# Kernel tuning notes

Hardware: AMD Instinct MI355X
Metric: run time of the kernel (lower is better)

## Reference

```python
import jax, jax.numpy as jnp
import numpy as np

EMBED_DIM = 1024
NUM_HEADS = 16
HEAD_DIM = EMBED_DIM // NUM_HEADS
B, N = 4, 2048


def setup_inputs() -> dict:
    key = jax.random.key(0)
    k = jax.random.split(key, 5)
    s = 1.0 / np.sqrt(EMBED_DIM)
    return {
        "x": jax.random.normal(k[0], (B, N, EMBED_DIM), dtype=jnp.float32),
        "W_qkv": jax.random.uniform(k[1], (EMBED_DIM, 3 * EMBED_DIM), jnp.float32, -s, s),
        "b_qkv": jax.random.uniform(k[2], (3 * EMBED_DIM,), jnp.float32, -s, s),
        "W_proj": jax.random.uniform(k[3], (EMBED_DIM, EMBED_DIM), jnp.float32, -s, s),
        "b_proj": jax.random.uniform(k[4], (EMBED_DIM,), jnp.float32, -s, s),
    }


def reference(x, W_qkv, b_qkv, W_proj, b_proj):
    b, n, c = x.shape
    qkv = x @ W_qkv + b_qkv                       # [B,N,3C]
    qkv = qkv.reshape(b, n, 3, NUM_HEADS, HEAD_DIM)
    q = qkv[:, :, 0].transpose(0, 2, 1, 3)        # [B,H,N,D]
    k = qkv[:, :, 1].transpose(0, 2, 1, 3)
    v = qkv[:, :, 2].transpose(0, 2, 1, 3)
    scale = 1.0 / np.sqrt(HEAD_DIM).astype(np.float32)
    scores = jnp.einsum("bhqd,bhkd->bhqk", q, k) * scale
    attn = jax.nn.softmax(scores, axis=-1)
    out = jnp.einsum("bhqk,bhkd->bhqd", attn, v)  # [B,H,N,D]
    out = out.transpose(0, 2, 1, 3).reshape(b, n, c)
    return out @ W_proj + b_proj
```

## Files before the change

### kernel.cpp

```cpp
#include <hip/hip_runtime.h>
#include <math.h>


typedef __bf16 bf16x8 __attribute__((ext_vector_type(8)));
typedef float f32x4 __attribute__((ext_vector_type(4)));

#define EMBED 1024
#define NHEAD 16
#define BATCH 4
#define SEQ 2048
#define M_TOT 8192
#define QKV_N 3072
#define QSCALE 0.18033688011112042f

__device__ __forceinline__ ushort f2bf(float f) {
  union { float f; unsigned u; } x; x.f = f;
  unsigned r = x.u + 0x7FFFu + ((x.u >> 16) & 1u);
  return (ushort)(r >> 16);
}

__device__ __forceinline__ uint cvt2bf(float a, float b) {
#if __has_builtin(__builtin_amdgcn_cvt_pk_bf16_f32)
  typedef __bf16 bf16x2 __attribute__((ext_vector_type(2)));
  union { bf16x2 v; uint u; } c;
  c.v = __builtin_amdgcn_cvt_pk_bf16_f32(a, b);
  return c.u;
#else
  return (uint)f2bf(a) | ((uint)f2bf(b) << 16);
#endif
}

__device__ __forceinline__ f32x4 mfma16(bf16x8 a, bf16x8 b, f32x4 c) {
  return __builtin_amdgcn_mfma_f32_16x16x32_bf16(a, b, c, 0, 0, 0);
}

__device__ __forceinline__ void gl2lds16(const void* g, void* l) {
  __builtin_amdgcn_global_load_lds(
      (const __attribute__((address_space(1))) unsigned int*)g,
      (__attribute__((address_space(3))) unsigned int*)l, 16, 0, 0);
}

__global__ __launch_bounds__(256) void cvt_f32_bf16(
    const float* __restrict__ in, ushort* __restrict__ out) {
  int i = (blockIdx.x * 256 + threadIdx.x) * 4;
  float4 v = *reinterpret_cast<const float4*>(&in[i]);
  uint2 w = {cvt2bf(v.x, v.y), cvt2bf(v.z, v.w)};
  *reinterpret_cast<uint2*>(&out[i]) = w;
}

__global__ __launch_bounds__(256) void transpose_to_bf16(
    const float* __restrict__ in, ushort* __restrict__ out, int Kd, int Nd) {
  __shared__ float tile[64][65];
  const int t = threadIdx.x;
  const int n0 = blockIdx.x * 64, k0 = blockIdx.y * 64;
#pragma unroll
  for (int i = 0; i < 16; ++i) {
    int e = t + 256 * i;
    int kr = e >> 6, nc = e & 63;
    tile[kr][nc] = in[(size_t)(k0 + kr) * Nd + n0 + nc];
  }
  __syncthreads();
#pragma unroll
  for (int i = 0; i < 16; ++i) {
    int e = t + 256 * i;
    int nr = e >> 6, kc = e & 63;
    out[(size_t)(n0 + nr) * Kd + k0 + kc] = f2bf(tile[kc][nr]);
  }
}

__global__ __launch_bounds__(256) void gemm_bf16(
    const ushort* __restrict__ A, const ushort* __restrict__ Bt,
    const float* __restrict__ bias, void* __restrict__ Cout,
    ushort* __restrict__ vtgout, int M, int N, int K, int mode) {
  __shared__ ushort As[128 * 32];
  __shared__ ushort Bs[128 * 32];
  const int t = threadIdx.x;
  const int wave = t >> 6, lane = t & 63;
  const int lane15 = lane & 15, quad = lane >> 4;
  const int m0 = blockIdx.y * 128, n0 = blockIdx.x * 128;
  const int wm = (wave >> 1) * 64, wn = (wave & 1) * 64;

  int srow[2], scol[2], sdst[2];
#pragma unroll
  for (int j = 0; j < 2; ++j) {
    int c = (j * 4 + wave) * 64 + lane;
    int row = c >> 2;
    scol[j] = (((c & 3) ^ ((row >> 1) & 3)) * 8);
    srow[j] = row;
    sdst[j] = (j * 4 + wave) * 512;
  }
  const int swG = (lane15 >> 1) & 3;

  f32x4 acc[4][4] = {};

  for (int k0 = 0; k0 < K; k0 += 32) {
#pragma unroll
    for (int j = 0; j < 2; ++j) {
      gl2lds16(&A[(size_t)(m0 + srow[j]) * K + k0 + scol[j]], &As[sdst[j]]);
      gl2lds16(&Bt[(size_t)(n0 + srow[j]) * K + k0 + scol[j]], &Bs[sdst[j]]);
    }
    __syncthreads();

    bf16x8 af[4], bfr[4];
#pragma unroll
    for (int ms = 0; ms < 4; ++ms)
      af[ms] = *reinterpret_cast<const bf16x8*>(
          &As[(wm + ms * 16 + lane15) * 32 + ((quad ^ swG) * 8)]);
#pragma unroll
    for (int ns = 0; ns < 4; ++ns)
      bfr[ns] = *reinterpret_cast<const bf16x8*>(
          &Bs[(wn + ns * 16 + lane15) * 32 + ((quad ^ swG) * 8)]);
#pragma unroll
    for (int ms = 0; ms < 4; ++ms)
#pragma unroll
      for (int ns = 0; ns < 4; ++ns)
        acc[ms][ns] = mfma16(af[ms], bfr[ns], acc[ms][ns]);
    __syncthreads();
  }

  if (mode == 0) {
    float* out = (float*)Cout;
#pragma unroll
    for (int ns = 0; ns < 4; ++ns) {
      int col = n0 + wn + ns * 16 + lane15;
      float bv = bias[col];
#pragma unroll
      for (int ms = 0; ms < 4; ++ms)
#pragma unroll
        for (int r = 0; r < 4; ++r) {
          int row = m0 + wm + ms * 16 + quad * 4 + r;
          out[(size_t)row * N + col] = acc[ms][ns][r] + bv;
        }
    }
  } else {
    ushort* qk = (ushort*)Cout;
#pragma unroll
    for (int ns = 0; ns < 4; ++ns) {
      int col = n0 + wn + ns * 16 + lane15;
      float bv = bias[col];
      if (col < 2048) {
        float sc = (col < 1024) ? QSCALE : 1.0f;
#pragma unroll
        for (int ms = 0; ms < 4; ++ms) {
          int row = m0 + wm + ms * 16 + quad * 4;
          uint u01 = cvt2bf((acc[ms][ns][0] + bv) * sc, (acc[ms][ns][1] + bv) * sc);
          uint u23 = cvt2bf((acc[ms][ns][2] + bv) * sc, (acc[ms][ns][3] + bv) * sc);
          qk[(size_t)(row + 0) * 2048 + col] = (ushort)u01;
          qk[(size_t)(row + 1) * 2048 + col] = (ushort)(u01 >> 16);
          qk[(size_t)(row + 2) * 2048 + col] = (ushort)u23;
          qk[(size_t)(row + 3) * 2048 + col] = (ushort)(u23 >> 16);
        }
      } else {
        int dp = col - 2048;
#pragma unroll
        for (int ms = 0; ms < 4; ++ms) {
          int row = m0 + wm + ms * 16 + quad * 4;
          int b = row >> 11, seq = row & 2047;
          uint2 w = {cvt2bf(acc[ms][ns][0] + bv, acc[ms][ns][1] + bv),
                     cvt2bf(acc[ms][ns][2] + bv, acc[ms][ns][3] + bv)};
          *reinterpret_cast<uint2*>(
              &vtgout[((size_t)(b * 1024 + dp) << 11) + seq]) = w;
        }
      }
    }
  }
}

#define APD 72
#define QG 4

__global__ __launch_bounds__(256, 2) void attn_kernel(
    const ushort* __restrict__ qk, const ushort* __restrict__ vtg,
    ushort* __restrict__ out) {
  __shared__ ushort Ks[2][4096];
  __shared__ ushort Vt[2][4096];
  __shared__ ushort Ps[4][16 * APD];

  const int t = threadIdx.x;
  const int wave = t >> 6, lane = t & 63;
  const int lane15 = lane & 15, quad = lane >> 4;
  const int bh = blockIdx.x, qg = blockIdx.y;
  const int b = bh >> 4, h = bh & 15;
  const size_t boff = (size_t)b * SEQ * 2048;

  int sdst[2];
  const ushort* kptr[2];
  const ushort* vptr[2];
#pragma unroll
  for (int j = 0; j < 2; ++j) {
    int lg = (j * 4 + wave) * 64 + lane;
    int row = lg >> 3;
    int col = ((lg & 7) ^ (row & 7)) * 8;
    sdst[j] = (j * 4 + wave) * 512;
    kptr[j] = qk + boff + (size_t)row * 2048 + 1024 + h * 64 + col;
    vptr[j] = vtg + ((size_t)(b * 1024 + h * 64 + row) << 11) + col;
  }

  bf16x8 qf[QG][2];
#pragma unroll
  for (int g = 0; g < QG; ++g) {
    size_t qoff =
        boff + (size_t)(qg * 256 + g * 64 + wave * 16 + lane15) * 2048 + h * 64;
    qf[g][0] = *reinterpret_cast<const bf16x8*>(&qk[qoff + quad * 8]);
    qf[g][1] = *reinterpret_cast<const bf16x8*>(&qk[qoff + 32 + quad * 8]);
  }

  bf16x8 ones;
#pragma unroll
  for (int j = 0; j < 8; ++j) ones[j] = (__bf16)1.0f;

  f32x4 O[QG][4] = {};
  f32x4 lacc[QG] = {};
  const int sw = lane15 & 7;
  ushort* ps = Ps[wave];

#pragma unroll
  for (int j = 0; j < 2; ++j) {
    gl2lds16(kptr[j], &Ks[0][sdst[j]]);
    gl2lds16(vptr[j], &Vt[0][sdst[j]]);
  }
  __syncthreads();

  for (int kt = 0; kt < SEQ / 64; ++kt) {
    const int cur = kt & 1, nxt = cur ^ 1;
    if (kt < SEQ / 64 - 1) {
#pragma unroll
      for (int j = 0; j < 2; ++j) {
        gl2lds16(kptr[j] + (size_t)(kt + 1) * 64 * 2048, &Ks[nxt][sdst[j]]);
        gl2lds16(vptr[j] + (kt + 1) * 64, &Vt[nxt][sdst[j]]);
      }
    }

    bf16x8 kf[4][2], vf[2][4];
#pragma unroll
    for (int nsub = 0; nsub < 4; ++nsub) {
      const int kr = (nsub * 16 + lane15) * 64;
      kf[nsub][0] = *reinterpret_cast<const bf16x8*>(
          &Ks[cur][kr + ((quad ^ sw) * 8)]);
      kf[nsub][1] = *reinterpret_cast<const bf16x8*>(
          &Ks[cur][kr + (((quad + 4) ^ sw) * 8)]);
    }
#pragma unroll
    for (int kk = 0; kk < 2; ++kk)
#pragma unroll
      for (int dsub = 0; dsub < 4; ++dsub) {
        int d = dsub * 16 + lane15;
        vf[kk][dsub] = *reinterpret_cast<const bf16x8*>(
            &Vt[cur][d * 64 + (((kk * 4 + quad) ^ sw) * 8)]);
      }

#pragma unroll
    for (int g = 0; g < QG; ++g) {
      f32x4 st[4];
#pragma unroll
      for (int nsub = 0; nsub < 4; ++nsub) {
        f32x4 a = {-32.0f, -32.0f, -32.0f, -32.0f};
        a = mfma16(kf[nsub][0], qf[g][0], a);
        a = mfma16(kf[nsub][1], qf[g][1], a);
        st[nsub] = a;
      }
#pragma unroll
      for (int nsub = 0; nsub < 4; ++nsub) {
        uint2 w = {cvt2bf(exp2f(st[nsub][0]), exp2f(st[nsub][1])),
                   cvt2bf(exp2f(st[nsub][2]), exp2f(st[nsub][3]))};
        *reinterpret_cast<uint2*>(
            &ps[lane15 * APD + nsub * 16 + quad * 4]) = w;
      }
#pragma unroll
      for (int kk = 0; kk < 2; ++kk) {
        bf16x8 pf = *reinterpret_cast<const bf16x8*>(
            &ps[lane15 * APD + kk * 32 + quad * 8]);
#pragma unroll
        for (int dsub = 0; dsub < 4; ++dsub)
          O[g][dsub] = mfma16(pf, vf[kk][dsub], O[g][dsub]);
        lacc[g] = mfma16(pf, ones, lacc[g]);
      }
    }
    __syncthreads();
  }

#pragma unroll
  for (int g = 0; g < QG; ++g)
#pragma unroll
    for (int r = 0; r < 4; ++r) {
      float linv = __builtin_amdgcn_rcpf(lacc[g][r]);
      size_t rowoff =
          (size_t)(b * SEQ + qg * 256 + g * 64 + wave * 16 + quad * 4 + r) *
              EMBED + h * 64;
      uint u01 = cvt2bf(O[g][0][r] * linv, O[g][1][r] * linv);
      uint u23 = cvt2bf(O[g][2][r] * linv, O[g][3][r] * linv);
      out[rowoff + 0 * 16 + lane15] = (ushort)u01;
      out[rowoff + 1 * 16 + lane15] = (ushort)(u01 >> 16);
      out[rowoff + 2 * 16 + lane15] = (ushort)u23;
      out[rowoff + 3 * 16 + lane15] = (ushort)(u23 >> 16);
    }
}

extern "C" void kernel_launch(void* const* d_in, const int* in_sizes, int n_in,
                              void* d_out, int out_size, void* d_ws,
                              size_t ws_size, hipStream_t stream) {
  const float* x = (const float*)d_in[0];
  const float* Wqkv = (const float*)d_in[1];
  const float* bqkv = (const float*)d_in[2];
  const float* Wproj = (const float*)d_in[3];
  const float* bproj = (const float*)d_in[4];
  float* out = (float*)d_out;

  char* ws = (char*)d_ws;
  ushort* Wqkv_t = (ushort*)ws;
  ushort* Wproj_t = (ushort*)(ws + 6291456);
  ushort* qk = (ushort*)(ws + 8388608);
  ushort* vtg = (ushort*)(ws + 41943040);
  ushort* xb = (ushort*)(ws + 58720256);
  ushort* attnout = (ushort*)(ws + 58720256);

  cvt_f32_bf16<<<M_TOT * EMBED / 1024, 256, 0, stream>>>(x, xb);
  transpose_to_bf16<<<dim3(QKV_N / 64, EMBED / 64), 256, 0, stream>>>(
      Wqkv, Wqkv_t, EMBED, QKV_N);
  transpose_to_bf16<<<dim3(EMBED / 64, EMBED / 64), 256, 0, stream>>>(
      Wproj, Wproj_t, EMBED, EMBED);
  gemm_bf16<<<dim3(QKV_N / 128, M_TOT / 128), 256, 0, stream>>>(
      xb, Wqkv_t, bqkv, qk, vtg, M_TOT, QKV_N, EMBED, 1);
  attn_kernel<<<dim3(NHEAD * BATCH, SEQ / 256), 256, 0, stream>>>(
      qk, vtg, attnout);
  gemm_bf16<<<dim3(EMBED / 128, M_TOT / 128), 256, 0, stream>>>(
      attnout, Wproj_t, bproj, out, nullptr, M_TOT, EMBED, EMBED, 0);
}
```

Baseline: 314.1 us.

## Halve attention query groups per block, raise occupancy, swizzle P tile, load V inline

Cuts the query groups per attention block from 4 to 2, doubling the grid and raising launch bounds to 4 blocks per CU. V fragments are now read from LDS inside the PV loop instead of held in registers, and the P scratch tile drops its padding for an XOR swizzle. exp2f is replaced by the hardware exp2 builtin. The aim is more occupancy and lower register pressure, at the cost of more K/V tile loads across blocks and repeated V LDS reads per query group.

```diff
diff --git a/kernel.cpp b/kernel.cpp
--- a/kernel.cpp
+++ b/kernel.cpp
@@ -27,6 +27,14 @@
   return c.u;
 #else
   return (uint)f2bf(a) | ((uint)f2bf(b) << 16);
+#endif
+}
+
+__device__ __forceinline__ float fexp2(float x) {
+#if __has_builtin(__builtin_amdgcn_exp2f)
+  return __builtin_amdgcn_exp2f(x);
+#else
+  return exp2f(x);
 #endif
 }
 
@@ -166,15 +174,14 @@
   }
 }
 
-#define APD 72
-#define QG 4
-
-__global__ __launch_bounds__(256, 2) void attn_kernel(
+#define QG 2
+
+__global__ __launch_bounds__(256, 4) void attn_kernel(
     const ushort* __restrict__ qk, const ushort* __restrict__ vtg,
     ushort* __restrict__ out) {
   __shared__ ushort Ks[2][4096];
   __shared__ ushort Vt[2][4096];
-  __shared__ ushort Ps[4][16 * APD];
+  __shared__ ushort Ps[4][16 * 64];
 
   const int t = threadIdx.x;
   const int wave = t >> 6, lane = t & 63;
@@ -199,8 +206,8 @@
   bf16x8 qf[QG][2];
 #pragma unroll
   for (int g = 0; g < QG; ++g) {
-    size_t qoff =
-        boff + (size_t)(qg * 256 + g * 64 + wave * 16 + lane15) * 2048 + h * 64;
+    size_t qoff = boff +
+        (size_t)(qg * (QG * 64) + g * 64 + wave * 16 + lane15) * 2048 + h * 64;
     qf[g][0] = *reinterpret_cast<const bf16x8*>(&qk[qoff + quad * 8]);
     qf[g][1] = *reinterpret_cast<const bf16x8*>(&qk[qoff + 32 + quad * 8]);
   }
@@ -231,7 +238,7 @@
       }
     }
 
-    bf16x8 kf[4][2], vf[2][4];
+    bf16x8 kf[4][2];
 #pragma unroll
     for (int nsub = 0; nsub < 4; ++nsub) {
       const int kr = (nsub * 16 + lane15) * 64;
@@ -240,14 +247,6 @@
       kf[nsub][1] = *reinterpret_cast<const bf16x8*>(
           &Ks[cur][kr + (((quad + 4) ^ sw) * 8)]);
     }
-#pragma unroll
-    for (int kk = 0; kk < 2; ++kk)
-#pragma unroll
-      for (int dsub = 0; dsub < 4; ++dsub) {
-        int d = dsub * 16 + lane15;
-        vf[kk][dsub] = *reinterpret_cast<const bf16x8*>(
-            &Vt[cur][d * 64 + (((kk * 4 + quad) ^ sw) * 8)]);
-      }
 
 #pragma unroll
     for (int g = 0; g < QG; ++g) {
@@ -261,18 +260,23 @@
       }
 #pragma unroll
       for (int nsub = 0; nsub < 4; ++nsub) {
-        uint2 w = {cvt2bf(exp2f(st[nsub][0]), exp2f(st[nsub][1])),
-                   cvt2bf(exp2f(st[nsub][2]), exp2f(st[nsub][3]))};
+        uint2 w = {cvt2bf(fexp2(st[nsub][0]), fexp2(st[nsub][1])),
+                   cvt2bf(fexp2(st[nsub][2]), fexp2(st[nsub][3]))};
         *reinterpret_cast<uint2*>(
-            &ps[lane15 * APD + nsub * 16 + quad * 4]) = w;
+            &ps[lane15 * 64 + (((2 * nsub + (quad >> 1)) ^ sw) << 3) +
+                ((quad & 1) << 2)]) = w;
       }
 #pragma unroll
       for (int kk = 0; kk < 2; ++kk) {
         bf16x8 pf = *reinterpret_cast<const bf16x8*>(
-            &ps[lane15 * APD + kk * 32 + quad * 8]);
-#pragma unroll
-        for (int dsub = 0; dsub < 4; ++dsub)
-          O[g][dsub] = mfma16(pf, vf[kk][dsub], O[g][dsub]);
+            &ps[lane15 * 64 + (((kk * 4 + quad) ^ sw) << 3)]);
+#pragma unroll
+        for (int dsub = 0; dsub < 4; ++dsub) {
+          int d = dsub * 16 + lane15;
+          bf16x8 vf = *reinterpret_cast<const bf16x8*>(
+              &Vt[cur][d * 64 + (((kk * 4 + quad) ^ sw) * 8)]);
+          O[g][dsub] = mfma16(pf, vf, O[g][dsub]);
+        }
         lacc[g] = mfma16(pf, ones, lacc[g]);
       }
     }
@@ -285,8 +289,8 @@
     for (int r = 0; r < 4; ++r) {
       float linv = __builtin_amdgcn_rcpf(lacc[g][r]);
       size_t rowoff =
-          (size_t)(b * SEQ + qg * 256 + g * 64 + wave * 16 + quad * 4 + r) *
-              EMBED + h * 64;
+          (size_t)(b * SEQ + qg * (QG * 64) + g * 64 + wave * 16 + quad * 4 +
+                   r) * EMBED + h * 64;
       uint u01 = cvt2bf(O[g][0][r] * linv, O[g][1][r] * linv);
       uint u23 = cvt2bf(O[g][2][r] * linv, O[g][3][r] * linv);
       out[rowoff + 0 * 16 + lane15] = (ushort)u01;
@@ -321,7 +325,7 @@
       Wproj, Wproj_t, EMBED, EMBED);
   gemm_bf16<<<dim3(QKV_N / 128, M_TOT / 128), 256, 0, stream>>>(
       xb, Wqkv_t, bqkv, qk, vtg, M_TOT, QKV_N, EMBED, 1);
-  attn_kernel<<<dim3(NHEAD * BATCH, SEQ / 256), 256, 0, stream>>>(
+  attn_kernel<<<dim3(NHEAD * BATCH, SEQ / (QG * 64)), 256, 0, stream>>>(
       qk, vtg, attnout);
   gemm_bf16<<<dim3(EMBED / 128, M_TOT / 128), 256, 0, stream>>>(
       attnout, Wproj_t, bproj, out, nullptr, M_TOT, EMBED, EMBED, 0);
```

Result: no change. 310.5 us (-1.2%).
